# Kernel optimization log

Measured on AMD Instinct MI355X. Metric: run time of the kernel, lower is better.

Reference implementation:

```python
import jax, jax.numpy as jnp
import numpy as np

NUM_GROUPS = 32
EPS = 1e-6


def setup_inputs() -> dict:
    key = jax.random.key(0)
    ks = jax.random.split(key, 6)
    n, t, c, h, w = 2, 5, 64, 128, 128
    K = 512  # codebook size
    return {
        "x": jax.random.normal(ks[0], (n, t, c, h, w), dtype=jnp.float32),
        "mb": jax.random.normal(ks[1], (c, K), dtype=jnp.float32),
        "phi_w": jax.random.normal(ks[2], (c, c), dtype=jnp.float32) * (1.0 / np.sqrt(c)),
        "phi_b": jax.random.normal(ks[3], (c,), dtype=jnp.float32) * 0.01,
        "gn_w": jnp.ones((c,), dtype=jnp.float32),
        "gn_b": jnp.zeros((c,), dtype=jnp.float32),
        "wz_w": jax.random.normal(ks[4], (c, c), dtype=jnp.float32) * (1.0 / np.sqrt(c)),
        "wz_b": jax.random.normal(ks[5], (c,), dtype=jnp.float32) * 0.01,
    }


def reference(x, mb, phi_w, phi_b, gn_w, gn_b, wz_w, wz_b):
    n, t, c, h, w = x.shape
    B = n * t
    xf = x.reshape(B, c, h, w)

    # GroupNorm(32 groups, eps=1e-6, affine)
    xg = xf.reshape(B, NUM_GROUPS, c // NUM_GROUPS, h, w)
    mu = jnp.mean(xg, axis=(2, 3, 4), keepdims=True)
    var = jnp.var(xg, axis=(2, 3, 4), keepdims=True)
    xn = ((xg - mu) * jax.lax.rsqrt(var + EPS)).reshape(B, c, h, w)
    xn = xn * gn_w[:, None, None] + gn_b[:, None, None]

    # 1x1 conv phi, flatten spatial -> tokens (B, HW, C)
    phi = jnp.einsum('oc,bchw->bohw', phi_w, xn) + phi_b[:, None, None]
    p = phi.reshape(B, c, h * w).transpose(0, 2, 1)

    # soft-VQ attention against codebook mb (C, K)
    scores = jnp.einsum('bnc,ck->bnk', p, mb) * (c ** -0.5)
    attn = jax.nn.softmax(scores, axis=-1)
    y = jnp.einsum('bnk,ck->bnc', attn, mb)  # (B, HW, C)

    y = y.transpose(0, 2, 1).reshape(B, c, h, w)
    out = jnp.einsum('oc,bchw->bohw', wz_w, y) + wz_b[:, None, None] + xf
    return out.reshape(n, t, c, h, w)
```

## Files before the change

### kernel.cpp

```cpp
#include <hip/hip_runtime.h>


#define HWN 16384
#define CCH 64
#define PSC 0.18033688011112042f

using short8 = __attribute__((ext_vector_type(8))) short;
using f32x4  = __attribute__((ext_vector_type(4))) float;

__device__ __forceinline__ ushort f2bf(float f) {
    union { float f; unsigned int i; } v; v.f = f;
    return (ushort)((v.i + 0x8000u) >> 16);
}
__device__ __forceinline__ unsigned int pk2(float a, float b) {
    union { float f; unsigned int i; } va, vb; va.f = a; vb.f = b;
    return __builtin_amdgcn_perm(vb.i + 0x8000u, va.i + 0x8000u, 0x07060302u);
}

__global__ __launch_bounds__(256) void prep_stats_kernel(
    const float* __restrict__ x, const float* __restrict__ mb,
    const float* __restrict__ phiw, const float* __restrict__ wzw,
    ushort* __restrict__ ws, int nstat)
{
    if (blockIdx.x >= nstat) {
        int i = (blockIdx.x - nstat) * 256 + threadIdx.x;
        int j = i & 7, lane = (i >> 3) & 63, m = lane & 15, q = lane >> 4;
        if (i < 32768) {
            int t = i >> 9, tile = t >> 1, s = t & 1;
            ws[i] = f2bf(mb[(s * 32 + q * 8 + j) * 512 + tile * 16 + m]);
        } else if (i < 65536) {
            int t = (i - 32768) >> 9;
            int mt = t & 3, u2 = t >> 2, s2 = u2 & 1, cc = u2 >> 1;
            ws[i] = f2bf(mb[(mt * 16 + m) * 512 + cc * 64 + s2 * 32 + q * 8 + j]);
        } else if (i < 69632) {
            int t = (i - 65536) >> 9, mt = t >> 1, s = t & 1;
            ws[i] = f2bf(phiw[(mt * 16 + m) * 64 + s * 32 + q * 8 + j]);
        } else {
            int t = (i - 69632) >> 9, mt = t >> 1, s = t & 1;
            ws[i] = f2bf(wzw[(mt * 16 + m) * 64 + s * 32 + q * 8 + j]);
        }
        return;
    }
    float* statf = (float*)(ws + 73728);
    int blk  = blockIdx.x;
    int b    = blk >> 8;
    int g    = (blk >> 3) & 31;
    int part = blk & 7;
    const float4* b4 = (const float4*)(x + (size_t)b * CCH * HWN + (size_t)(g * 2) * HWN) + part * 1024;
    float s = 0.f, s2 = 0.f;
    for (int i = threadIdx.x; i < 1024; i += 256) {
        float4 u = b4[i];
        s  += (u.x + u.y) + (u.z + u.w);
        s2 += (u.x*u.x + u.y*u.y) + (u.z*u.z + u.w*u.w);
    }
    for (int off = 32; off > 0; off >>= 1) {
        s  += __shfl_down(s, off);
        s2 += __shfl_down(s2, off);
    }
    __shared__ float rs[4], rs2[4];
    int wave = threadIdx.x >> 6, lane = threadIdx.x & 63;
    if (lane == 0) { rs[wave] = s; rs2[wave] = s2; }
    __syncthreads();
    if (threadIdx.x == 0) {
        atomicAdd(&statf[b * 32 + g],       rs[0] + rs[1] + rs[2] + rs[3]);
        atomicAdd(&statf[320 + b * 32 + g], rs2[0] + rs2[1] + rs2[2] + rs2[3]);
    }
}

__global__ __launch_bounds__(128, 2) void main_mfma(
    const float* __restrict__ x, const ushort* __restrict__ ws,
    const float* __restrict__ phib, const float* __restrict__ gnw,
    const float* __restrict__ gnb, const float* __restrict__ wzb,
    float* __restrict__ out)
{
    const int lane = threadIdx.x & 63, wv = threadIdx.x >> 6;
    const int m = lane & 15, q = lane >> 4;
    const int blk = blockIdx.x;
    const int b   = blk >> 8;
    const int hw0 = ((blk & 255) << 6) + (wv << 5);

    const ushort* mbA  = ws;
    const ushort* mbY  = ws + 32768;
    const ushort* phiA = ws + 65536;
    const ushort* wzA  = ws + 69632;
    const float*  statf = (const float*)(ws + 73728);

    __shared__ ushort Sl[2][2][32 * 72];
    ushort* Ebuf[2] = { &Sl[wv][0][0], &Sl[wv][1][0] };
    ushort* E0 = Ebuf[0];

    const float* xb = x + (size_t)b * CCH * HWN;

    short8 bx[2][2];
#pragma unroll
    for (int s = 0; s < 2; ++s) {
        const int cbase = s * 32 + q * 8;
        f32x4 sm4 = *(const f32x4*)(statf + b * 32 + (cbase >> 1));
        f32x4 sq4 = *(const f32x4*)(statf + 320 + b * 32 + (cbase >> 1));
        f32x4 mu4, rs4;
#pragma unroll
        for (int r = 0; r < 4; ++r) {
            mu4[r] = sm4[r] * (1.f / 32768.f);
            float var = sq4[r] * (1.f / 32768.f) - mu4[r] * mu4[r];
            rs4[r] = rsqrtf(var + 1e-6f);
        }
        f32x4 gwv0 = *(const f32x4*)(gnw + cbase), gwv1 = *(const f32x4*)(gnw + cbase + 4);
        f32x4 gbv0 = *(const f32x4*)(gnb + cbase), gbv1 = *(const f32x4*)(gnb + cbase + 4);
#pragma unroll
        for (int n = 0; n < 2; ++n)
#pragma unroll
        for (int j = 0; j < 8; ++j) {
            float v  = xb[(size_t)(cbase + j) * HWN + hw0 + n * 16 + m];
            float gw = (j < 4) ? gwv0[j & 3] : gwv1[j & 3];
            float gb = (j < 4) ? gbv0[j & 3] : gbv1[j & 3];
            float xn = (v - mu4[j >> 1]) * rs4[j >> 1] * gw + gb;
            bx[n][s][j] = (short)f2bf(xn);
        }
    }

#pragma unroll
    for (int mt = 0; mt < 4; ++mt) {
        f32x4 a[2];
#pragma unroll
        for (int n = 0; n < 2; ++n) a[n] = (f32x4){0.f,0.f,0.f,0.f};
#pragma unroll
        for (int s = 0; s < 2; ++s) {
            short8 ap = *(const short8*)(phiA + (((mt * 2 + s) * 64 + lane) << 3));
#pragma unroll
            for (int n = 0; n < 2; ++n)
                a[n] = __builtin_amdgcn_mfma_f32_16x16x32_bf16(ap, bx[n][s], a[n], 0, 0, 0);
        }
        f32x4 pb = *(const f32x4*)(phib + mt * 16 + q * 4);
#pragma unroll
        for (int n = 0; n < 2; ++n)
            *(uint2*)(E0 + (n * 16 + m) * 72 + mt * 16 + q * 4) =
                make_uint2(pk2((a[n][0]+pb[0])*PSC, (a[n][1]+pb[1])*PSC),
                           pk2((a[n][2]+pb[2])*PSC, (a[n][3]+pb[3])*PSC));
    }

    short8 bp[2][2];
#pragma unroll
    for (int n = 0; n < 2; ++n)
#pragma unroll
    for (int s = 0; s < 2; ++s)
        bp[n][s] = *(const short8*)(E0 + (n * 16 + m) * 72 + s * 32 + q * 8);

    f32x4 accY[2][4];
#pragma unroll
    for (int n = 0; n < 2; ++n)
#pragma unroll
    for (int mt = 0; mt < 4; ++mt) accY[n][mt] = (f32x4){0.f,0.f,0.f,0.f};
    float lsum[2] = {0.f, 0.f};

    for (int cc = 0; cc < 8; ++cc) {
        ushort* Eb = Ebuf[cc & 1];
#pragma unroll
        for (int u = 0; u < 4; ++u) {
            short8 am0 = *(const short8*)(mbA + ((((cc * 4 + u) * 2 + 0) * 64 + lane) << 3));
            short8 am1 = *(const short8*)(mbA + ((((cc * 4 + u) * 2 + 1) * 64 + lane) << 3));
#pragma unroll
            for (int n = 0; n < 2; ++n) {
                f32x4 sa = {0.f,0.f,0.f,0.f};
                sa = __builtin_amdgcn_mfma_f32_16x16x32_bf16(am0, bp[n][0], sa, 0, 0, 0);
                sa = __builtin_amdgcn_mfma_f32_16x16x32_bf16(am1, bp[n][1], sa, 0, 0, 0);
                float e0 = __builtin_exp2f(sa[0]), e1 = __builtin_exp2f(sa[1]);
                float e2 = __builtin_exp2f(sa[2]), e3 = __builtin_exp2f(sa[3]);
                lsum[n] += (e0 + e1) + (e2 + e3);
                *(uint2*)(Eb + (n * 16 + m) * 72 + u * 16 + q * 4) =
                    make_uint2(pk2(e0, e1), pk2(e2, e3));
            }
        }
#pragma unroll
        for (int s2 = 0; s2 < 2; ++s2) {
            short8 be[2];
#pragma unroll
            for (int n = 0; n < 2; ++n)
                be[n] = *(const short8*)(Eb + (n * 16 + m) * 72 + s2 * 32 + q * 8);
#pragma unroll
            for (int mt = 0; mt < 4; ++mt) {
                short8 ay = *(const short8*)(mbY + ((((cc * 2 + s2) * 4 + mt) * 64 + lane) << 3));
#pragma unroll
                for (int n = 0; n < 2; ++n)
                    accY[n][mt] = __builtin_amdgcn_mfma_f32_16x16x32_bf16(ay, be[n], accY[n][mt], 0, 0, 0);
            }
        }
    }

    float linv[2];
#pragma unroll
    for (int n = 0; n < 2; ++n) {
        float l = lsum[n];
        l += __shfl_xor(l, 16);
        l += __shfl_xor(l, 32);
        linv[n] = 1.f / l;
    }

#pragma unroll
    for (int mt = 0; mt < 4; ++mt)
#pragma unroll
    for (int n = 0; n < 2; ++n)
        *(uint2*)(E0 + (n * 16 + m) * 72 + mt * 16 + q * 4) =
            make_uint2(pk2(accY[n][mt][0], accY[n][mt][1]), pk2(accY[n][mt][2], accY[n][mt][3]));

    short8 by[2][2];
#pragma unroll
    for (int n = 0; n < 2; ++n)
#pragma unroll
    for (int s = 0; s < 2; ++s)
        by[n][s] = *(const short8*)(E0 + (n * 16 + m) * 72 + s * 32 + q * 8);

    float* ob = out + (size_t)b * CCH * HWN;
#pragma unroll
    for (int mt = 0; mt < 4; ++mt) {
        f32x4 c[2];
#pragma unroll
        for (int n = 0; n < 2; ++n) c[n] = (f32x4){0.f,0.f,0.f,0.f};
#pragma unroll
        for (int s = 0; s < 2; ++s) {
            short8 aw = *(const short8*)(wzA + (((mt * 2 + s) * 64 + lane) << 3));
#pragma unroll
            for (int n = 0; n < 2; ++n)
                c[n] = __builtin_amdgcn_mfma_f32_16x16x32_bf16(aw, by[n][s], c[n], 0, 0, 0);
        }
        f32x4 wb = *(const f32x4*)(wzb + mt * 16 + q * 4);
#pragma unroll
        for (int r = 0; r < 4; ++r) {
            int o = mt * 16 + q * 4 + r;
            size_t base = (size_t)o * HWN + hw0 + m;
#pragma unroll
            for (int n = 0; n < 2; ++n)
                ob[base + n * 16] = c[n][r] * linv[n] + wb[r] + xb[base + n * 16];
        }
    }
}

extern "C" void kernel_launch(void* const* d_in, const int* in_sizes, int n_in,
                              void* d_out, int out_size, void* d_ws, size_t ws_size,
                              hipStream_t stream) {
    const float* x    = (const float*)d_in[0];
    const float* mb   = (const float*)d_in[1];
    const float* phiw = (const float*)d_in[2];
    const float* phib = (const float*)d_in[3];
    const float* gnw  = (const float*)d_in[4];
    const float* gnb  = (const float*)d_in[5];
    const float* wzw  = (const float*)d_in[6];
    const float* wzb  = (const float*)d_in[7];

    const int B = in_sizes[0] / (CCH * HWN);
    const int nstat = B * 256;

    hipMemsetAsync((char*)d_ws + 36864 * 4, 0, 640 * 4, stream);
    prep_stats_kernel<<<nstat + 288, 256, 0, stream>>>(x, mb, phiw, wzw,
                                                       (ushort*)d_ws, nstat);
    main_mfma<<<B * 256, 128, 0, stream>>>(x, (const ushort*)d_ws,
                                           phib, gnw, gnb, wzb, (float*)d_out);
}
```

Baseline: 172.6 us.

## Stage codebook fragments into LDS with async loads shared across four waves

Blocks grow from two to four waves, and the codebook MFMA fragments are streamed into a four-slot LDS ring with global_load_lds, double-buffered ahead of use. Before, each wave read them straight from global/L2. The per-wave score/exp buffers shrink to 32-wide half chunks (stride 40). The Y-accumulation MFMAs run at raised wave priority. This cuts redundant global codebook traffic per wave, at the cost of block-wide barriers every iteration and more LDS per block, which may limit occupancy.

```diff
diff --git a/kernel.cpp b/kernel.cpp
--- a/kernel.cpp
+++ b/kernel.cpp
@@ -4,6 +4,7 @@
 #define HWN 16384
 #define CCH 64
 #define PSC 0.18033688011112042f
+#define ETS 40
 
 using short8 = __attribute__((ext_vector_type(8))) short;
 using f32x4  = __attribute__((ext_vector_type(4))) float;
@@ -67,7 +68,20 @@
     }
 }
 
-__global__ __launch_bounds__(128, 2) void main_mfma(
+__device__ __forceinline__ void stage_chunk(const ushort* ws, ushort* fg,
+                                            int hc, int wv, int lane) {
+    const char* g = (const char*)ws + (wv >= 2 ? 65536 : 0) + hc * 4096
+                    + (wv & 1) * 2048 + lane * 16;
+    char* l = (char*)fg + (wv >= 2 ? 4096 : 0) + (wv & 1) * 2048 + lane * 16;
+#pragma unroll
+    for (int k = 0; k < 2; ++k)
+        __builtin_amdgcn_global_load_lds(
+            (const __attribute__((address_space(1))) unsigned int*)(g + k * 1024),
+            (__attribute__((address_space(3))) unsigned int*)(l + k * 1024),
+            16, 0, 0);
+}
+
+__global__ __launch_bounds__(256, 2) void main_mfma(
     const float* __restrict__ x, const ushort* __restrict__ ws,
     const float* __restrict__ phib, const float* __restrict__ gnw,
     const float* __restrict__ gnb, const float* __restrict__ wzb,
@@ -76,20 +90,21 @@
     const int lane = threadIdx.x & 63, wv = threadIdx.x >> 6;
     const int m = lane & 15, q = lane >> 4;
     const int blk = blockIdx.x;
-    const int b   = blk >> 8;
-    const int hw0 = ((blk & 255) << 6) + (wv << 5);
-
-    const ushort* mbA  = ws;
-    const ushort* mbY  = ws + 32768;
+    const int b   = blk >> 7;
+    const int hw0 = ((blk & 127) << 7) + (wv << 5);
+
     const ushort* phiA = ws + 65536;
     const ushort* wzA  = ws + 69632;
     const float*  statf = (const float*)(ws + 73728);
 
-    __shared__ ushort Sl[2][2][32 * 72];
+    __shared__ ushort Fg[4][4096];
+    __shared__ ushort Sl[4][2][32 * ETS];
     ushort* Ebuf[2] = { &Sl[wv][0][0], &Sl[wv][1][0] };
-    ushort* E0 = Ebuf[0];
 
     const float* xb = x + (size_t)b * CCH * HWN;
+
+    stage_chunk(ws, &Fg[0][0], 0, wv, lane);
+    stage_chunk(ws, &Fg[1][0], 1, wv, lane);
 
     short8 bx[2][2];
 #pragma unroll
@@ -133,7 +148,7 @@
         f32x4 pb = *(const f32x4*)(phib + mt * 16 + q * 4);
 #pragma unroll
         for (int n = 0; n < 2; ++n)
-            *(uint2*)(E0 + (n * 16 + m) * 72 + mt * 16 + q * 4) =
+            *(uint2*)(Ebuf[mt >> 1] + (n * 16 + m) * ETS + (mt & 1) * 16 + q * 4) =
                 make_uint2(pk2((a[n][0]+pb[0])*PSC, (a[n][1]+pb[1])*PSC),
                            pk2((a[n][2]+pb[2])*PSC, (a[n][3]+pb[3])*PSC));
     }
@@ -143,7 +158,10 @@
     for (int n = 0; n < 2; ++n)
 #pragma unroll
     for (int s = 0; s < 2; ++s)
-        bp[n][s] = *(const short8*)(E0 + (n * 16 + m) * 72 + s * 32 + q * 8);
+        bp[n][s] = *(const short8*)(Ebuf[s] + (n * 16 + m) * ETS + q * 8);
+
+    asm volatile("s_waitcnt vmcnt(0)" ::: "memory");
+    __builtin_amdgcn_s_barrier();
 
     f32x4 accY[2][4];
 #pragma unroll
@@ -152,37 +170,54 @@
     for (int mt = 0; mt < 4; ++mt) accY[n][mt] = (f32x4){0.f,0.f,0.f,0.f};
     float lsum[2] = {0.f, 0.f};
 
-    for (int cc = 0; cc < 8; ++cc) {
-        ushort* Eb = Ebuf[cc & 1];
-#pragma unroll
-        for (int u = 0; u < 4; ++u) {
-            short8 am0 = *(const short8*)(mbA + ((((cc * 4 + u) * 2 + 0) * 64 + lane) << 3));
-            short8 am1 = *(const short8*)(mbA + ((((cc * 4 + u) * 2 + 1) * 64 + lane) << 3));
-#pragma unroll
-            for (int n = 0; n < 2; ++n) {
-                f32x4 sa = {0.f,0.f,0.f,0.f};
-                sa = __builtin_amdgcn_mfma_f32_16x16x32_bf16(am0, bp[n][0], sa, 0, 0, 0);
-                sa = __builtin_amdgcn_mfma_f32_16x16x32_bf16(am1, bp[n][1], sa, 0, 0, 0);
-                float e0 = __builtin_exp2f(sa[0]), e1 = __builtin_exp2f(sa[1]);
-                float e2 = __builtin_exp2f(sa[2]), e3 = __builtin_exp2f(sa[3]);
-                lsum[n] += (e0 + e1) + (e2 + e3);
-                *(uint2*)(Eb + (n * 16 + m) * 72 + u * 16 + q * 4) =
-                    make_uint2(pk2(e0, e1), pk2(e2, e3));
+    for (int iv = 0; iv < 8; ++iv) {
+        if (iv < 7) {
+            stage_chunk(ws, &Fg[(2 * iv + 2) & 3][0], 2 * iv + 2, wv, lane);
+            stage_chunk(ws, &Fg[(2 * iv + 3) & 3][0], 2 * iv + 3, wv, lane);
+        }
+#pragma unroll
+        for (int h = 0; h < 2; ++h) {
+            const int hc = 2 * iv + h;
+            const ushort* fA = &Fg[hc & 3][0];
+            ushort* Eb = Ebuf[h];
+#pragma unroll
+            for (int u = 0; u < 2; ++u) {
+                short8 am0 = *(const short8*)(fA + (((u * 2 + 0) * 64 + lane) << 3));
+                short8 am1 = *(const short8*)(fA + (((u * 2 + 1) * 64 + lane) << 3));
+#pragma unroll
+                for (int n = 0; n < 2; ++n) {
+                    f32x4 sa = (f32x4){0.f,0.f,0.f,0.f};
+                    sa = __builtin_amdgcn_mfma_f32_16x16x32_bf16(am0, bp[n][0], sa, 0, 0, 0);
+                    sa = __builtin_amdgcn_mfma_f32_16x16x32_bf16(am1, bp[n][1], sa, 0, 0, 0);
+                    float e0 = __builtin_exp2f(sa[0]), e1 = __builtin_exp2f(sa[1]);
+                    float e2 = __builtin_exp2f(sa[2]), e3 = __builtin_exp2f(sa[3]);
+                    lsum[n] += (e0 + e1) + (e2 + e3);
+                    *(uint2*)(Eb + (n * 16 + m) * ETS + u * 16 + q * 4) =
+                        make_uint2(pk2(e0, e1), pk2(e2, e3));
+                }
             }
         }
-#pragma unroll
-        for (int s2 = 0; s2 < 2; ++s2) {
+        __builtin_amdgcn_s_setprio(1);
+#pragma unroll
+        for (int h = 0; h < 2; ++h) {
+            const int hc = 2 * iv + h;
+            const ushort* fY = &Fg[hc & 3][0] + 2048;
             short8 be[2];
 #pragma unroll
             for (int n = 0; n < 2; ++n)
-                be[n] = *(const short8*)(Eb + (n * 16 + m) * 72 + s2 * 32 + q * 8);
+                be[n] = *(const short8*)(Ebuf[h] + (n * 16 + m) * ETS + q * 8);
 #pragma unroll
             for (int mt = 0; mt < 4; ++mt) {
-                short8 ay = *(const short8*)(mbY + ((((cc * 2 + s2) * 4 + mt) * 64 + lane) << 3));
+                short8 ay = *(const short8*)(fY + ((mt * 64 + lane) << 3));
 #pragma unroll
                 for (int n = 0; n < 2; ++n)
                     accY[n][mt] = __builtin_amdgcn_mfma_f32_16x16x32_bf16(ay, be[n], accY[n][mt], 0, 0, 0);
             }
+        }
+        __builtin_amdgcn_s_setprio(0);
+        if (iv < 7) {
+            asm volatile("s_waitcnt vmcnt(0)" ::: "memory");
+            __builtin_amdgcn_s_barrier();
         }
     }
 
@@ -198,16 +233,17 @@
 #pragma unroll
     for (int mt = 0; mt < 4; ++mt)
 #pragma unroll
+        for (int n = 0; n < 2; ++n)
+            *(uint2*)(Ebuf[mt >> 1] + (n * 16 + m) * ETS + (mt & 1) * 16 + q * 4) =
+                make_uint2(pk2(accY[n][mt][0], accY[n][mt][1]),
+                           pk2(accY[n][mt][2], accY[n][mt][3]));
+
+    short8 by[2][2];
+#pragma unroll
     for (int n = 0; n < 2; ++n)
-        *(uint2*)(E0 + (n * 16 + m) * 72 + mt * 16 + q * 4) =
-            make_uint2(pk2(accY[n][mt][0], accY[n][mt][1]), pk2(accY[n][mt][2], accY[n][mt][3]));
-
-    short8 by[2][2];
-#pragma unroll
-    for (int n = 0; n < 2; ++n)
 #pragma unroll
     for (int s = 0; s < 2; ++s)
-        by[n][s] = *(const short8*)(E0 + (n * 16 + m) * 72 + s * 32 + q * 8);
+        by[n][s] = *(const short8*)(Ebuf[s] + (n * 16 + m) * ETS + q * 8);
 
     float* ob = out + (size_t)b * CCH * HWN;
 #pragma unroll
@@ -252,6 +288,6 @@
     hipMemsetAsync((char*)d_ws + 36864 * 4, 0, 640 * 4, stream);
     prep_stats_kernel<<<nstat + 288, 256, 0, stream>>>(x, mb, phiw, wzw,
                                                        (ushort*)d_ws, nstat);
-    main_mfma<<<B * 256, 128, 0, stream>>>(x, (const ushort*)d_ws,
+    main_mfma<<<B * 128, 256, 0, stream>>>(x, (const ushort*)d_ws,
                                            phib, gnw, gnb, wzb, (float*)d_out);
 }
```

New measurement: 149.5 us. 1.15x faster.
